# Optimization experiments

Measured on AMD Instinct MI355X. Metric: run time of the kernel, lower is better.

Reference implementation:

```python
import jax, jax.numpy as jnp
import numpy as np


def setup_inputs() -> dict:
    key = jax.random.key(0)
    k1, k2 = jax.random.split(key)
    B, N, C = 2, 1024, 64  # batch_size, block_num, out_channels
    regional_means = jax.random.normal(k1, (B, N, C), dtype=jnp.float32)
    # nn.Parameter randn then kaiming_uniform_: just use scaled random weights
    W = jax.random.normal(k2, (C, C), dtype=jnp.float32) * (1.0 / np.sqrt(C))
    return {"regional_means": regional_means, "W": W, "c": C}


def reference(regional_means, W, c):
    # regional_means: (B, N, c); W: (c, c)
    B, N, _ = regional_means.shape
    M = W @ W.T  # (c, c), PSD Mahalanobis metric
    # pairwise differences diff[b, i, j] = means[b, i] - means[b, j]  -> (B, N, N, c)
    # (original materializes this via repeat/permute; sign flip from its final
    #  permute is irrelevant since the quadratic form is even)
    diff = regional_means[:, :, None, :] - regional_means[:, None, :, :]
    # quadratic form q[b,i,j] = diff^T M diff
    q = jnp.einsum('bijc,cd,bijd->bij', diff, M, diff)
    adj = jnp.exp(-q) + jnp.eye(N, dtype=regional_means.dtype)[None, :, :]
    return adj
```

## Files before the change

kernel.cpp:

```cpp
#include <hip/hip_runtime.h>
#include <hip/hip_bf16.h>
#include <math.h>


typedef __attribute__((ext_vector_type(8))) short bf16x8;
typedef __attribute__((ext_vector_type(4))) float f32x4;

__global__ void __launch_bounds__(256) y_kernel(
    const float* __restrict__ X, const float* __restrict__ W,
    __hip_bfloat16* __restrict__ Y, float* __restrict__ r)
{
    __shared__ float Ws[64][64];
    __shared__ float Xs[4][64];

    const int t = threadIdx.x;
    const float4* W4 = (const float4*)W;
    float4* Ws4 = (float4*)&Ws[0][0];
#pragma unroll
    for (int c = 0; c < 4; ++c) Ws4[c * 256 + t] = W4[c * 256 + t];

    const int row0 = blockIdx.x * 4;
    const int rr = t >> 6;
    const int lane = t & 63;
    Xs[rr][lane] = X[(size_t)(row0 + rr) * 64 + lane];
    __syncthreads();

    float y = 0.f;
#pragma unroll
    for (int k = 0; k < 64; ++k)
        y = fmaf(Xs[rr][k], Ws[k][lane], y);

    const __hip_bfloat16 yb = __float2bfloat16(y);
    Y[(size_t)(row0 + rr) * 64 + lane] = yb;

    const float yf = __bfloat162float(yb);
    float s = yf * yf;
#pragma unroll
    for (int off = 32; off > 0; off >>= 1) s += __shfl_down(s, off, 64);
    if (lane == 0) r[row0 + rr] = s;
}

__global__ void __launch_bounds__(256) gram_kernel(
    const __hip_bfloat16* __restrict__ Y, const float* __restrict__ r,
    float* __restrict__ out, int N)
{
    const int t = threadIdx.x;
    const int wave = t >> 6, lane = t & 63;
    const int tpr = N >> 4;
    const int tile = blockIdx.x * 4 + wave;
    const int it = tile / tpr, jt = tile % tpr;
    const int b  = blockIdx.z;

    const int ib = it << 4, jb = jt << 4;
    const unsigned short* Yb = (const unsigned short*)Y + (size_t)b * N * 64;
    const float* rb = r + (size_t)b * N;

    const int m  = lane & 15;
    const int k0 = (lane >> 4) * 8;

    const bf16x8 a0 = *(const bf16x8*)(Yb + (size_t)(ib + m) * 64 + k0);
    const bf16x8 a1 = *(const bf16x8*)(Yb + (size_t)(ib + m) * 64 + k0 + 32);
    const bf16x8 b0 = *(const bf16x8*)(Yb + (size_t)(jb + m) * 64 + k0);
    const bf16x8 b1 = *(const bf16x8*)(Yb + (size_t)(jb + m) * 64 + k0 + 32);

    f32x4 acc = {0.f, 0.f, 0.f, 0.f};
    acc = __builtin_amdgcn_mfma_f32_16x16x32_bf16(a0, b0, acc, 0, 0, 0);
    acc = __builtin_amdgcn_mfma_f32_16x16x32_bf16(a1, b1, acc, 0, 0, 0);

    const int gj = jb + m;
    const float rjv = rb[gj];
    const size_t obase = (size_t)b * N * N;
    const int quad4 = (lane >> 4) * 4;
#pragma unroll
    for (int v = 0; v < 4; ++v) {
        const int gi = ib + quad4 + v;
        float q = rb[gi] + rjv - 2.f * acc[v];
        float val = __expf(-q);
        if (gi == gj) val += 1.f;
        out[obase + (size_t)gi * N + gj] = val;
    }
}

extern "C" void kernel_launch(void* const* d_in, const int* in_sizes, int n_in,
                              void* d_out, int out_size, void* d_ws, size_t ws_size,
                              hipStream_t stream) {
    const float* X = (const float*)d_in[0];
    const float* W = (const float*)d_in[1];
    float* out = (float*)d_out;

    const int C  = 64;
    const int BN = in_sizes[0] / C;
    const int N  = (int)(((long long)out_size * C) / in_sizes[0]);
    const int B  = BN / N;

    __hip_bfloat16* Ybf = (__hip_bfloat16*)d_ws;
    float* r = (float*)((char*)d_ws + (size_t)BN * C * sizeof(__hip_bfloat16));

    y_kernel<<<BN / 4, 256, 0, stream>>>(X, W, Ybf, r);

    const int tpr = N >> 4;
    gram_kernel<<<dim3((tpr * tpr) / 4, 1, B), 256, 0, stream>>>(Ybf, r, out, N);
}
```

Before: 66.17 us.

## Fuse projection and Gram computation into one MFMA kernel with 64x64 tiles

Replaces the two-kernel pipeline (Y = XW projection, then a 16x16-tile Gram) with a single kernel. Each block handles a 64x64 output tile and recomputes the bf16 projection of its row and column slabs with MFMA in shared memory. This removes one launch and the workspace round trip, and reuses each Y slab across four output subtiles. The cost is redundant Y recomputation in every block, plus W and X quantised to bf16 before the projection, which loses precision compared with the previous fp32 projection.

```diff
diff --git a/kernel.cpp b/kernel.cpp
--- a/kernel.cpp
+++ b/kernel.cpp
@@ -6,84 +6,124 @@
 typedef __attribute__((ext_vector_type(8))) short bf16x8;
 typedef __attribute__((ext_vector_type(4))) float f32x4;
 
-__global__ void __launch_bounds__(256) y_kernel(
+#define PITCH 72
+
+static __device__ __forceinline__ void store4bf(__hip_bfloat16* p, float4 v) {
+    __hip_bfloat16 h[4] = {__float2bfloat16(v.x), __float2bfloat16(v.y),
+                           __float2bfloat16(v.z), __float2bfloat16(v.w)};
+    *(uint2*)p = *(const uint2*)h;
+}
+
+__global__ void __launch_bounds__(256, 2) adj_fused_mfma(
     const float* __restrict__ X, const float* __restrict__ W,
-    __hip_bfloat16* __restrict__ Y, float* __restrict__ r)
+    float* __restrict__ out, int N)
 {
-    __shared__ float Ws[64][64];
-    __shared__ float Xs[4][64];
+    __shared__ __hip_bfloat16 sXi[64][PITCH];
+    __shared__ __hip_bfloat16 sXj[64][PITCH];
+    __shared__ __hip_bfloat16 sWT[64][PITCH];
+    __shared__ __hip_bfloat16 sYi[64][PITCH];
+    __shared__ __hip_bfloat16 sYj[64][PITCH];
+    __shared__ float rs[2][64];
 
-    const int t = threadIdx.x;
-    const float4* W4 = (const float4*)W;
-    float4* Ws4 = (float4*)&Ws[0][0];
+    const int b    = blockIdx.z;
+    const int ib   = blockIdx.y << 6;
+    const int jb   = blockIdx.x << 6;
+    const bool diag = (ib == jb);
+    const int t    = threadIdx.x;
+    const int wave = t >> 6;
+    const int lane = t & 63;
+    const int m    = lane & 15;
+    const int q    = lane >> 4;
+    const int r16  = wave << 4;
+
+    const float* __restrict__ Xb = X + (size_t)b * N * 64;
+
+    const float4* W4  = (const float4*)W;
+    const float4* Xi4 = (const float4*)(Xb + (size_t)ib * 64);
+    const float4* Xj4 = (const float4*)(Xb + (size_t)jb * 64);
 #pragma unroll
-    for (int c = 0; c < 4; ++c) Ws4[c * 256 + t] = W4[c * 256 + t];
-
-    const int row0 = blockIdx.x * 4;
-    const int rr = t >> 6;
-    const int lane = t & 63;
-    Xs[rr][lane] = X[(size_t)(row0 + rr) * 64 + lane];
+    for (int it = 0; it < 4; ++it) {
+        const int idx = it * 256 + t;
+        const int row = idx >> 4;
+        const int c4  = (idx & 15) << 2;
+        const float4 wv = W4[idx];
+        sWT[c4 + 0][row] = __float2bfloat16(wv.x);
+        sWT[c4 + 1][row] = __float2bfloat16(wv.y);
+        sWT[c4 + 2][row] = __float2bfloat16(wv.z);
+        sWT[c4 + 3][row] = __float2bfloat16(wv.w);
+        store4bf(&sXi[row][c4], Xi4[idx]);
+        if (!diag) store4bf(&sXj[row][c4], Xj4[idx]);
+    }
     __syncthreads();
 
-    float y = 0.f;
+    auto computeY = [&](const __hip_bfloat16 (*sX)[PITCH],
+                        __hip_bfloat16 (*sY)[PITCH], float* rdst) {
+        const bf16x8 a0 = *(const bf16x8*)&sX[r16 + m][q * 8];
+        const bf16x8 a1 = *(const bf16x8*)&sX[r16 + m][q * 8 + 32];
+        float p[4] = {0.f, 0.f, 0.f, 0.f};
 #pragma unroll
-    for (int k = 0; k < 64; ++k)
-        y = fmaf(Xs[rr][k], Ws[k][lane], y);
+        for (int ci = 0; ci < 4; ++ci) {
+            const bf16x8 b0 = *(const bf16x8*)&sWT[(ci << 4) + m][q * 8];
+            const bf16x8 b1 = *(const bf16x8*)&sWT[(ci << 4) + m][q * 8 + 32];
+            f32x4 acc = {0.f, 0.f, 0.f, 0.f};
+            acc = __builtin_amdgcn_mfma_f32_16x16x32_bf16(a0, b0, acc, 0, 0, 0);
+            acc = __builtin_amdgcn_mfma_f32_16x16x32_bf16(a1, b1, acc, 0, 0, 0);
+#pragma unroll
+            for (int v = 0; v < 4; ++v) {
+                const __hip_bfloat16 hb = __float2bfloat16(acc[v]);
+                sY[r16 + q * 4 + v][(ci << 4) + m] = hb;
+                const float f = __bfloat162float(hb);
+                p[v] = fmaf(f, f, p[v]);
+            }
+        }
+#pragma unroll
+        for (int off = 1; off < 16; off <<= 1)
+#pragma unroll
+            for (int v = 0; v < 4; ++v) p[v] += __shfl_xor(p[v], off, 64);
+        if (m == 0)
+#pragma unroll
+            for (int v = 0; v < 4; ++v) rdst[r16 + q * 4 + v] = p[v];
+    };
 
-    const __hip_bfloat16 yb = __float2bfloat16(y);
-    Y[(size_t)(row0 + rr) * 64 + lane] = yb;
+    computeY(sXi, sYi, rs[0]);
+    if (!diag) computeY(sXj, sYj, rs[1]);
+    __syncthreads();
 
-    const float yf = __bfloat162float(yb);
-    float s = yf * yf;
+    const __hip_bfloat16 (*pYj)[PITCH] = diag ? sYi : sYj;
+    const float* prj = diag ? rs[0] : rs[1];
+
+    const bf16x8 ga0 = *(const bf16x8*)&sYi[r16 + m][q * 8];
+    const bf16x8 ga1 = *(const bf16x8*)&sYi[r16 + m][q * 8 + 32];
+
+    const size_t obase = (size_t)b * N * N;
+    float ri[4];
 #pragma unroll
-    for (int off = 32; off > 0; off >>= 1) s += __shfl_down(s, off, 64);
-    if (lane == 0) r[row0 + rr] = s;
-}
+    for (int v = 0; v < 4; ++v) ri[v] = rs[0][r16 + q * 4 + v];
 
-__global__ void __launch_bounds__(256) gram_kernel(
-    const __hip_bfloat16* __restrict__ Y, const float* __restrict__ r,
-    float* __restrict__ out, int N)
-{
-    const int t = threadIdx.x;
-    const int wave = t >> 6, lane = t & 63;
-    const int tpr = N >> 4;
-    const int tile = blockIdx.x * 4 + wave;
-    const int it = tile / tpr, jt = tile % tpr;
-    const int b  = blockIdx.z;
-
-    const int ib = it << 4, jb = jt << 4;
-    const unsigned short* Yb = (const unsigned short*)Y + (size_t)b * N * 64;
-    const float* rb = r + (size_t)b * N;
-
-    const int m  = lane & 15;
-    const int k0 = (lane >> 4) * 8;
-
-    const bf16x8 a0 = *(const bf16x8*)(Yb + (size_t)(ib + m) * 64 + k0);
-    const bf16x8 a1 = *(const bf16x8*)(Yb + (size_t)(ib + m) * 64 + k0 + 32);
-    const bf16x8 b0 = *(const bf16x8*)(Yb + (size_t)(jb + m) * 64 + k0);
-    const bf16x8 b1 = *(const bf16x8*)(Yb + (size_t)(jb + m) * 64 + k0 + 32);
-
-    f32x4 acc = {0.f, 0.f, 0.f, 0.f};
-    acc = __builtin_amdgcn_mfma_f32_16x16x32_bf16(a0, b0, acc, 0, 0, 0);
-    acc = __builtin_amdgcn_mfma_f32_16x16x32_bf16(a1, b1, acc, 0, 0, 0);
-
-    const int gj = jb + m;
-    const float rjv = rb[gj];
-    const size_t obase = (size_t)b * N * N;
-    const int quad4 = (lane >> 4) * 4;
 #pragma unroll
-    for (int v = 0; v < 4; ++v) {
-        const int gi = ib + quad4 + v;
-        float q = rb[gi] + rjv - 2.f * acc[v];
-        float val = __expf(-q);
-        if (gi == gj) val += 1.f;
-        out[obase + (size_t)gi * N + gj] = val;
+    for (int mj = 0; mj < 4; ++mj) {
+        const bf16x8 gb0 = *(const bf16x8*)&pYj[(mj << 4) + m][q * 8];
+        const bf16x8 gb1 = *(const bf16x8*)&pYj[(mj << 4) + m][q * 8 + 32];
+        f32x4 acc = {0.f, 0.f, 0.f, 0.f};
+        acc = __builtin_amdgcn_mfma_f32_16x16x32_bf16(ga0, gb0, acc, 0, 0, 0);
+        acc = __builtin_amdgcn_mfma_f32_16x16x32_bf16(ga1, gb1, acc, 0, 0, 0);
+        const int gj = jb + (mj << 4) + m;
+        const float rjv = prj[(mj << 4) + m];
+#pragma unroll
+        for (int v = 0; v < 4; ++v) {
+            const int gi = ib + r16 + q * 4 + v;
+            const float qq = ri[v] + rjv - 2.f * acc[v];
+            float val = __expf(-qq);
+            if (gi == gj) val += 1.f;
+            out[obase + (size_t)gi * N + gj] = val;
+        }
     }
 }
 
 extern "C" void kernel_launch(void* const* d_in, const int* in_sizes, int n_in,
                               void* d_out, int out_size, void* d_ws, size_t ws_size,
                               hipStream_t stream) {
+    (void)n_in; (void)d_ws; (void)ws_size;
     const float* X = (const float*)d_in[0];
     const float* W = (const float*)d_in[1];
     float* out = (float*)d_out;
@@ -93,11 +133,5 @@
     const int N  = (int)(((long long)out_size * C) / in_sizes[0]);
     const int B  = BN / N;
 
-    __hip_bfloat16* Ybf = (__hip_bfloat16*)d_ws;
-    float* r = (float*)((char*)d_ws + (size_t)BN * C * sizeof(__hip_bfloat16));
-
-    y_kernel<<<BN / 4, 256, 0, stream>>>(X, W, Ybf, r);
-
-    const int tpr = N >> 4;
-    gram_kernel<<<dim3((tpr * tpr) / 4, 1, B), 256, 0, stream>>>(Ybf, r, out, N);
+    adj_fused_mfma<<<dim3(N / 64, N / 64, B), 256, 0, stream>>>(X, W, out, N);
 }
```

After: 63.51 us. 1.04x faster.
